# Kernel optimization log

Hardware: AMD Instinct MI355X
Metric: run time of the kernel (lower is better)

## Reference

```python
import jax, jax.numpy as jnp
import numpy as np

MIN_PS = 4
MAX_PS = 16


def _enforce(mb):
    # mb: (L,) bool candidate boundaries (merge_signal < 0.7-quantile)
    # Faithful re-implementation of _enforce_patch_size_constraints:
    # walk boundaries left->right, skip segments < MIN_PS (start not advanced),
    # accept otherwise, and insert ceil(ps/MAX_PS)-1 evenly spaced splits for
    # oversized segments. seq_len-1 is always appended as a candidate.
    L = mb.shape[0]
    pos = jnp.arange(L, dtype=jnp.int32)
    cand = mb | (pos == L - 1)

    def fwd_step(start, inp):
        p, is_c = inp
        ps = p - start
        acc = is_c & (ps >= MIN_PS)
        k = jnp.where(acc, (ps + MAX_PS - 1) // MAX_PS, jnp.int32(1))
        sz = jnp.maximum(jnp.where(acc, ps // k, jnp.int32(1)), 1)
        new_start = jnp.where(acc, p, start)
        return new_start, (acc, start, sz, k)

    _, (acc, seg_start, sz, k) = jax.lax.scan(fwd_step, jnp.int32(0), (pos, cand))

    # Reverse scan: propagate each accepted boundary's (start, split_size, num_splits)
    # back to the interior positions of its segment so splits can be placed in parallel.
    def rev_step(carry, inp):
        a, s, z, kk = inp
        cs, cz, ck, cv = carry
        out = (cs, cz, ck, cv)
        ncarry = (jnp.where(a, s, cs), jnp.where(a, z, cz), jnp.where(a, kk, ck), cv | a)
        return ncarry, out

    init = (jnp.int32(0), jnp.int32(1), jnp.int32(1), jnp.bool_(False))
    _, (fs, fz, fk, fv) = jax.lax.scan(rev_step, init, (acc, seg_start, sz, k), reverse=True)
    r = pos - fs
    j = r // fz
    split = fv & (r > 0) & (r % fz == 0) & (j >= 1) & (j <= fk - 1)
    return acc | split


def reference(x, attention_mask, W1, b1, W2, b2, Wc, bc, Wb1, bb1, Wb2, bb2):
    B, L, D = x.shape
    # content scorer: Linear -> ReLU -> Linear -> Sigmoid
    content = jax.nn.sigmoid(jax.nn.relu(x @ W1 + b1) @ W2 + b2)[..., 0]  # (B, L)
    # grouped Conv1d(d, d//2, k=3, pad=1, groups=d//4)
    xc = jnp.transpose(x, (0, 2, 1))  # (B, D, L)
    pf = jax.lax.conv_general_dilated(xc, Wc, (1,), ((1, 1),),
                                      feature_group_count=D // 4,
                                      dimension_numbers=('NCH', 'OIH', 'NCH'))
    pf = jnp.transpose(pf + bc[None, :, None], (0, 2, 1))  # (B, L, D//2)
    comb = jnp.concatenate([x, pf], axis=-1)
    bscore = jax.nn.sigmoid(jax.nn.relu(comb @ Wb1 + bb1) @ Wb2 + bb2)[..., 0]  # (B, L)
    signal = content * (1.0 - bscore) * attention_mask
    thr = jnp.quantile(signal, 0.7, axis=1, keepdims=True)
    mb = signal < thr
    new_b = jax.vmap(_enforce)(mb)  # (B, L) bool, new_b[:,0] is always False

    # segment id per token = inclusive cumsum of boundaries
    seg = jnp.cumsum(new_b.astype(jnp.int32), axis=1)
    seg_flat = (seg + jnp.arange(B, dtype=jnp.int32)[:, None] * L).reshape(-1)
    NS = B * L
    xm = x * attention_mask[..., None]
    e = jnp.sum(xm * xm, axis=-1).reshape(-1)  # softmax logits = ||token||^2
    m = jax.ops.segment_max(e, seg_flat, num_segments=NS)
    w = jnp.exp(e - m[seg_flat])
    denom = jax.ops.segment_sum(w, seg_flat, num_segments=NS)
    wn = w / denom[seg_flat]
    merged = jax.ops.segment_sum(xm.reshape(-1, D) * wn[:, None], seg_flat,
                                 num_segments=NS).reshape(B, L, D)
    # segment_boundaries: 1 for every segment except the first, zero padding
    n_last = seg[:, -1]
    p = jnp.arange(L)
    seg_bounds = ((p[None, :] >= 1) & (p[None, :] <= n_last[:, None])).astype(jnp.float32)
    return merged, seg_bounds


def setup_inputs() -> dict:
    key = jax.random.key(0)
    B, L, D = 4, 8192, 512
    ks = jax.random.split(key, 8)
    s = 0.02
    return {
        'x': jax.random.normal(ks[0], (B, L, D), jnp.float32),
        'attention_mask': jnp.ones((B, L), jnp.float32),
        'W1': jax.random.normal(ks[1], (D, D // 4), jnp.float32) * s,
        'b1': jnp.zeros((D // 4,), jnp.float32),
        'W2': jax.random.normal(ks[2], (D // 4, 1), jnp.float32) * s,
        'b2': jnp.zeros((1,), jnp.float32),
        'Wc': jax.random.normal(ks[3], (D // 2, 4, 3), jnp.float32) * s,
        'bc': jnp.zeros((D // 2,), jnp.float32),
        'Wb1': jax.random.normal(ks[4], (D + D // 2, D // 4), jnp.float32) * s,
        'bb1': jnp.zeros((D // 4,), jnp.float32),
        'Wb2': jax.random.normal(ks[5], (D // 4, 1), jnp.float32) * s,
        'bb2': jnp.zeros((1,), jnp.float32),
    }
```

## Files before the change

kernel.cpp:

```cpp
#include <hip/hip_runtime.h>
#include <math.h>

#define B_  4
#define L_  8192
#define D_  512
#define BL_ (B_*L_)
#define TOK 64
#define XS  68
#define KC  16
#define NCH (D_/KC)

__global__ __launch_bounds__(256, 2) void k_signal(
    const float* __restrict__ x, const float* __restrict__ mask,
    const float* __restrict__ W1, const float* __restrict__ b1,
    const float* __restrict__ W2, const float* __restrict__ b2,
    const float* __restrict__ Wc, const float* __restrict__ bc,
    const float* __restrict__ Wb1, const float* __restrict__ bb1,
    const float* __restrict__ Wb2, const float* __restrict__ bb2,
    float* __restrict__ signal, float* __restrict__ e)
{
  __shared__ float ws1[KC][128];
  __shared__ float wsb[KC][128];
  __shared__ float wsp[8][128];
  __shared__ float xt[KC][XS];
  __shared__ float pf[8][XS];

  const int t   = threadIdx.x;
  const int blk = blockIdx.x;
  const int b   = blk >> 7;
  const int l0  = (blk & 127) << 6;
  const float* xb = x + (size_t)b * L_ * D_;

  const int jq = t & 31, tw = t >> 5;
  const int j0 = jq << 2, tok0 = tw << 3;

  const int stok = t >> 2, skk = t & 3;
  const int oo_c = t >> 5;
  const int m2   = (t & 31) << 1;
  const int cb_c = (oo_c >> 1) << 2;

  const int srow = t >> 5, sc4 = (t & 31) << 2;

  float a1[8][4], a2[8][4];
#pragma unroll
  for (int i = 0; i < 8; ++i)
#pragma unroll
    for (int j = 0; j < 4; ++j) { a1[i][j] = 0.f; a2[i][j] = 0.f; }
  float esacc = 0.f;

  float4 r_w1a, r_w1b, r_wba, r_wbb, r_wp, r_xv, r_hv;
  float4 r_wc0, r_wc1, r_wc2;
  float  r_bc;

  auto LOAD = [&](int c) {
    const int kc = c << 4;
    r_w1a = *reinterpret_cast<const float4*>(W1  + (size_t)(kc + srow) * 128 + sc4);
    r_w1b = *reinterpret_cast<const float4*>(W1  + (size_t)(kc + 8 + srow) * 128 + sc4);
    r_wba = *reinterpret_cast<const float4*>(Wb1 + (size_t)(kc + srow) * 128 + sc4);
    r_wbb = *reinterpret_cast<const float4*>(Wb1 + (size_t)(kc + 8 + srow) * 128 + sc4);
    r_wp  = *reinterpret_cast<const float4*>(Wb1 + (size_t)(512 + (c << 3) + srow) * 128 + sc4);
    r_xv  = *reinterpret_cast<const float4*>(xb + (size_t)(l0 + stok) * D_ + kc + (skk << 2));
    if (t < 8) {
      const int hh = t >> 2, kk = t & 3;
      const int l = hh ? (l0 + TOK) : (l0 - 1);
      r_hv = make_float4(0.f, 0.f, 0.f, 0.f);
      if (l >= 0 && l < L_)
        r_hv = *reinterpret_cast<const float4*>(xb + (size_t)l * D_ + kc + (kk << 2));
    }
    const int o = (c << 3) + oo_c;
    const float* wcp = Wc + o * 12;
    r_wc0 = *reinterpret_cast<const float4*>(wcp);
    r_wc1 = *reinterpret_cast<const float4*>(wcp + 4);
    r_wc2 = *reinterpret_cast<const float4*>(wcp + 8);
    r_bc  = bc[o];
  };

  LOAD(0);

  for (int c = 0; c < NCH; ++c) {
    __syncthreads();

    *reinterpret_cast<float4*>(&ws1[srow][sc4])     = r_w1a;
    *reinterpret_cast<float4*>(&ws1[8 + srow][sc4]) = r_w1b;
    *reinterpret_cast<float4*>(&wsb[srow][sc4])     = r_wba;
    *reinterpret_cast<float4*>(&wsb[8 + srow][sc4]) = r_wbb;
    *reinterpret_cast<float4*>(&wsp[srow][sc4])     = r_wp;
    {
      const float4 v = r_xv;
      esacc = fmaf(v.x, v.x, esacc); esacc = fmaf(v.y, v.y, esacc);
      esacc = fmaf(v.z, v.z, esacc); esacc = fmaf(v.w, v.w, esacc);
      const int r = skk << 2;
      xt[r + 0][stok] = v.x; xt[r + 1][stok] = v.y;
      xt[r + 2][stok] = v.z; xt[r + 3][stok] = v.w;
    }
    if (t < 8) {
      const int hh = t >> 2, kk = t & 3;
      const int col = TOK + hh, r = kk << 2;
      xt[r + 0][col] = r_hv.x; xt[r + 1][col] = r_hv.y;
      xt[r + 2][col] = r_hv.z; xt[r + 3][col] = r_hv.w;
    }
    __syncthreads();

    float wcl[12];
    wcl[0] = r_wc0.x; wcl[1]  = r_wc0.y; wcl[2]  = r_wc0.z; wcl[3]  = r_wc0.w;
    wcl[4] = r_wc1.x; wcl[5]  = r_wc1.y; wcl[6]  = r_wc1.z; wcl[7]  = r_wc1.w;
    wcl[8] = r_wc2.x; wcl[9]  = r_wc2.y; wcl[10] = r_wc2.z; wcl[11] = r_wc2.w;
    const float bcv = r_bc;

    if (c + 1 < NCH) LOAD(c + 1);

    {
      float pa = bcv, pb = bcv;
      const int tm1 = (m2 == 0) ? TOK : m2 - 1;
      const int tp2 = (m2 + 2 == TOK) ? TOK + 1 : m2 + 2;
#pragma unroll
      for (int i = 0; i < 4; ++i) {
        const float* row = &xt[cb_c + i][0];
        const float  xm1 = row[tm1];
        const float2 x01 = *reinterpret_cast<const float2*>(&row[m2]);
        const float  xp2 = row[tp2];
        pa = fmaf(xm1,   wcl[i * 3 + 0], pa);
        pa = fmaf(x01.x, wcl[i * 3 + 1], pa);
        pa = fmaf(x01.y, wcl[i * 3 + 2], pa);
        pb = fmaf(x01.x, wcl[i * 3 + 0], pb);
        pb = fmaf(x01.y, wcl[i * 3 + 1], pb);
        pb = fmaf(xp2,   wcl[i * 3 + 2], pb);
      }
      *reinterpret_cast<float2*>(&pf[oo_c][m2]) = make_float2(pa, pb);
    }

#pragma unroll 4
    for (int k = 0; k < KC; ++k) {
      const float4 w1 = *reinterpret_cast<const float4*>(&ws1[k][j0]);
      const float4 wb = *reinterpret_cast<const float4*>(&wsb[k][j0]);
      const float4 xa = *reinterpret_cast<const float4*>(&xt[k][tok0]);
      const float4 xc = *reinterpret_cast<const float4*>(&xt[k][tok0 + 4]);
      const float xs8[8] = {xa.x, xa.y, xa.z, xa.w, xc.x, xc.y, xc.z, xc.w};
#pragma unroll
      for (int i = 0; i < 8; ++i) {
        a1[i][0] = fmaf(xs8[i], w1.x, a1[i][0]);
        a1[i][1] = fmaf(xs8[i], w1.y, a1[i][1]);
        a1[i][2] = fmaf(xs8[i], w1.z, a1[i][2]);
        a1[i][3] = fmaf(xs8[i], w1.w, a1[i][3]);
        a2[i][0] = fmaf(xs8[i], wb.x, a2[i][0]);
        a2[i][1] = fmaf(xs8[i], wb.y, a2[i][1]);
        a2[i][2] = fmaf(xs8[i], wb.z, a2[i][2]);
        a2[i][3] = fmaf(xs8[i], wb.w, a2[i][3]);
      }
    }
    __syncthreads();

#pragma unroll 2
    for (int oo = 0; oo < 8; ++oo) {
      const float4 wp = *reinterpret_cast<const float4*>(&wsp[oo][j0]);
      const float4 pa4 = *reinterpret_cast<const float4*>(&pf[oo][tok0]);
      const float4 pb4 = *reinterpret_cast<const float4*>(&pf[oo][tok0 + 4]);
      const float ps8[8] = {pa4.x, pa4.y, pa4.z, pa4.w, pb4.x, pb4.y, pb4.z, pb4.w};
#pragma unroll
      for (int i = 0; i < 8; ++i) {
        a2[i][0] = fmaf(ps8[i], wp.x, a2[i][0]);
        a2[i][1] = fmaf(ps8[i], wp.y, a2[i][1]);
        a2[i][2] = fmaf(ps8[i], wp.z, a2[i][2]);
        a2[i][3] = fmaf(ps8[i], wp.w, a2[i][3]);
      }
    }
  }

  {
    float b1v[4], w2v[4], bbv[4], wv2[4];
#pragma unroll
    for (int jj = 0; jj < 4; ++jj) {
      b1v[jj] = b1[j0 + jj];  w2v[jj] = W2[j0 + jj];
      bbv[jj] = bb1[j0 + jj]; wv2[jj] = Wb2[j0 + jj];
    }
    const float bias2 = b2[0], biasb2 = bb2[0];
#pragma unroll
    for (int i = 0; i < 8; ++i) {
      float p1 = 0.f, p2 = 0.f;
#pragma unroll
      for (int jj = 0; jj < 4; ++jj) {
        const float h1 = a1[i][jj] + b1v[jj];
        if (h1 > 0.f) p1 = fmaf(h1, w2v[jj], p1);
        const float h2 = a2[i][jj] + bbv[jj];
        if (h2 > 0.f) p2 = fmaf(h2, wv2[jj], p2);
      }
#pragma unroll
      for (int off = 1; off < 32; off <<= 1) {
        p1 += __shfl_xor(p1, off, 64);
        p2 += __shfl_xor(p2, off, 64);
      }
      if (jq == 0) {
        const int gi = b * L_ + l0 + tok0 + i;
        const float content = 1.f / (1.f + expf(-(p1 + bias2)));
        const float bscore  = 1.f / (1.f + expf(-(p2 + biasb2)));
        signal[gi] = content * (1.f - bscore) * mask[gi];
      }
    }
  }

  {
    float es = esacc;
    es += __shfl_xor(es, 1, 64);
    es += __shfl_xor(es, 2, 64);
    if (skk == 0) {
      const int gi = b * L_ + l0 + stok;
      const float m = mask[gi];
      e[gi] = m * m * es;
    }
  }
}

__device__ __forceinline__ int chain_sim(unsigned long long w, int from) {
  int last = -1;
  while (from < 64) {
    const unsigned long long m = w & (~0ull << from);
    if (m == 0ull) break;
    const int p = __ffsll(m) - 1;
    last = p;
    from = p + 4;
  }
  return last;
}

__global__ __launch_bounds__(1024) void k_select(
    const float* __restrict__ signal,
    int* __restrict__ starts, int* __restrict__ nlast, float* __restrict__ bounds)
{
  __shared__ unsigned int bins[4][256];
  __shared__ unsigned int sel_prefix;
  __shared__ int sel_rank;
  __shared__ float sh_thr;
  __shared__ unsigned int wmin[16];
  __shared__ int wcnt[16];
  __shared__ unsigned long long cw[128];
  __shared__ unsigned char nb[L_];
  __shared__ signed char tbl[128][4];
  __shared__ int st_in[128];
  __shared__ int tsum[256];
  __shared__ int offs[257];

  const int b = blockIdx.x, t = threadIdx.x;
  const int wv = t >> 6, lane = t & 63;
  const float* s = signal + b * L_;

  float val[8];
  unsigned int key[8];
#pragma unroll
  for (int i = 0; i < 8; ++i) {
    val[i] = s[(i << 10) + t];
    const unsigned int u = __float_as_uint(val[i]);
    key[i] = (u & 0x80000000u) ? ~u : (u | 0x80000000u);
  }

  if (t == 0) { sel_prefix = 0u; sel_rank = 5733; }
  __syncthreads();
  for (int round = 0; round < 4; ++round) {
    reinterpret_cast<unsigned int*>(bins)[t] = 0u;
    __syncthreads();
    const unsigned int pre = sel_prefix;
    const int shift = 24 - 8 * round;
#pragma unroll
    for (int i = 0; i < 8; ++i) {
      if (round == 0 || (key[i] >> (shift + 8)) == pre)
        atomicAdd(&bins[t >> 8][(key[i] >> shift) & 255u], 1u);
    }
    __syncthreads();
    if (t < 256)
      bins[0][t] = bins[0][t] + bins[1][t] + bins[2][t] + bins[3][t];
    __syncthreads();
    if (t < 64) {
      const unsigned int c0 = bins[0][(t << 2) + 0], c1 = bins[0][(t << 2) + 1];
      const unsigned int c2 = bins[0][(t << 2) + 2], c3 = bins[0][(t << 2) + 3];
      const unsigned int lsum = c0 + c1 + c2 + c3;
      unsigned int run = lsum;
#pragma unroll
      for (int off = 1; off < 64; off <<= 1) {
        const unsigned int v = __shfl_up(run, off, 64);
        if (t >= off) run += v;
      }
      const int r = sel_rank;
      if (r >= (int)(run - lsum) && r < (int)run) {
        int rr = r - (int)(run - lsum);
        unsigned int cbin;
        if (rr < (int)c0) { cbin = 0; }
        else if (rr < (int)(c0 + c1)) { cbin = 1; rr -= (int)c0; }
        else if (rr < (int)(c0 + c1 + c2)) { cbin = 2; rr -= (int)(c0 + c1); }
        else { cbin = 3; rr -= (int)(c0 + c1 + c2); }
        sel_rank = rr;
        sel_prefix = (pre << 8) | ((unsigned int)(t << 2) | cbin);
      }
    }
    __syncthreads();
  }
  const unsigned int k0 = sel_prefix;

  {
    int cle = 0;
    unsigned int mgt = 0xFFFFFFFFu;
#pragma unroll
    for (int i = 0; i < 8; ++i) {
      if (key[i] <= k0) ++cle;
      else mgt = min(mgt, key[i]);
    }
#pragma unroll
    for (int off = 1; off < 64; off <<= 1) {
      cle += __shfl_xor(cle, off, 64);
      mgt = min(mgt, (unsigned int)__shfl_xor((int)mgt, off, 64));
    }
    if (lane == 0) { wcnt[wv] = cle; wmin[wv] = mgt; }
    __syncthreads();
    if (t == 0) {
      int C = 0; unsigned int M = 0xFFFFFFFFu;
      for (int g = 0; g < 16; ++g) { C += wcnt[g]; M = min(M, wmin[g]); }
      const unsigned int k1 = (C >= 5735) ? k0 : M;
      const unsigned int u0 = (k0 & 0x80000000u) ? (k0 & 0x7fffffffu) : ~k0;
      const unsigned int u1 = (k1 & 0x80000000u) ? (k1 & 0x7fffffffu) : ~k1;
      const float v0 = __uint_as_float(u0);
      const float v1 = __uint_as_float(u1);
      const float g = 0.7f * 8191.0f - 5733.0f;
      sh_thr = v0 + g * (v1 - v0);
    }
    __syncthreads();
  }
  const float thr = sh_thr;

#pragma unroll
  for (int i = 0; i < 8; ++i) {
    const unsigned long long m = __ballot(val[i] < thr);
    if (lane == 0) cw[(i << 4) + wv] = m;
  }
  {
    const int base = t << 3;
#pragma unroll
    for (int i = 0; i < 8; ++i) nb[base + i] = 0;
  }
  __syncthreads();
  if (t == 0) cw[127] |= (1ull << 63);
  __syncthreads();

  if (t < 512) {
    const int blk = t >> 2, cls = t & 3;
    tbl[blk][cls] = (signed char)chain_sim(cw[blk], cls);
  }
  __syncthreads();

  if (t == 0) {
    int st = 0;
    for (int blk = 0; blk < 128; ++blk) {
      const int bs = blk << 6;
      st_in[blk] = st;
      int pl;
      if (blk == 0) {
        pl = chain_sim(cw[0], 4);
      } else {
        int off = st + 4 - bs;
        if (off < 0) off = 0;
        pl = tbl[blk][off];
      }
      if (pl >= 0) st = bs + pl;
    }
  }
  __syncthreads();

  if (t < 128) {
    const int bs = t << 6;
    const unsigned long long w = cw[t];
    int st = st_in[t];
    int from = st + 4 - bs;
    if (from < 0) from = 0;
    while (from < 64) {
      const unsigned long long m = w & (~0ull << from);
      if (m == 0ull) break;
      const int p_rel = __ffsll(m) - 1;
      const int p = bs + p_rel;
      nb[p] = 1;
      const int ps = p - st;
      const int k = (ps + 15) >> 4;
      if (k > 1) {
        int sz = ps / k; if (sz < 1) sz = 1;
        for (int j = 1; j < k; ++j) nb[st + j * sz] = 1;
      }
      st = p;
      from = p_rel + 4;
    }
  }
  __syncthreads();

  if (t < 256) {
    const int base = t << 5;
    int ls = 0;
    for (int i = 0; i < 32; ++i) ls += nb[base + i];
    tsum[t] = ls;
  }
  __syncthreads();
  if (t == 0) {
    int r = 0;
    for (int i = 0; i < 256; ++i) { offs[i] = r; r += tsum[i]; }
    offs[256] = r;
  }
  __syncthreads();
  if (t < 256) {
    const int base = t << 5;
    int run = offs[t];
    for (int i = 0; i < 32; ++i) {
      run += nb[base + i];
      if (nb[base + i]) starts[b * L_ + run] = base + i;
    }
  }
  if (t == 0) { starts[b * L_ + 0] = 0; nlast[b] = offs[256]; }
  __syncthreads();
  const int total = offs[256];
  for (int i = t; i < L_; i += 1024)
    bounds[b * L_ + i] = (i >= 1 && i <= total) ? 1.0f : 0.0f;
}

__global__ __launch_bounds__(256) void k_merge(const float* __restrict__ x,
    const float* __restrict__ mask, const float* __restrict__ e,
    const int* __restrict__ starts, const int* __restrict__ nlast,
    float* __restrict__ merged)
{
  const int idx = (blockIdx.x << 2) + (threadIdx.x >> 6);
  const int b   = idx >> 13;
  const int sid = idx & (L_ - 1);
  const int n = nlast[b];
  const int lane = threadIdx.x & 63;
  const int c0 = lane << 3;
  float* o = merged + (size_t)(b * L_ + sid) * D_ + c0;
  if (sid > n) {
    const float4 z = make_float4(0.f, 0.f, 0.f, 0.f);
    reinterpret_cast<float4*>(o)[0] = z;
    reinterpret_cast<float4*>(o)[1] = z;
    return;
  }
  const int t0 = starts[b * L_ + sid];
  const int t1 = (sid < n) ? starts[b * L_ + sid + 1] : L_;
  const int len = t1 - t0;
  const float* eb = e + b * L_;

  float acc[8] = {0,0,0,0,0,0,0,0};

  if (len <= 64) {
    const float ev = (lane < len) ? eb[t0 + lane] : -INFINITY;
    float mx = ev;
#pragma unroll
    for (int off = 1; off < 64; off <<= 1)
      mx = fmaxf(mx, __shfl_xor(mx, off, 64));
    const float ex = expf(ev - mx);
    float den = ex;
#pragma unroll
    for (int off = 1; off < 64; off <<= 1)
      den += __shfl_xor(den, off, 64);
    const float mk = (lane < len) ? mask[b * L_ + t0 + lane] : 0.f;
    const float scl = (ex / den) * mk;

    const float* xr = x + (size_t)(b * L_ + t0) * D_ + c0;
    float4 u0 = reinterpret_cast<const float4*>(xr)[0];
    float4 u1 = reinterpret_cast<const float4*>(xr)[1];
    for (int r = 0; r < len; ++r) {
      float4 n0, n1;
      if (r + 1 < len) {
        const float* xn = xr + (size_t)(r + 1) * D_;
        n0 = reinterpret_cast<const float4*>(xn)[0];
        n1 = reinterpret_cast<const float4*>(xn)[1];
      }
      const float sc = __shfl(scl, r, 64);
      acc[0] = fmaf(sc, u0.x, acc[0]); acc[1] = fmaf(sc, u0.y, acc[1]);
      acc[2] = fmaf(sc, u0.z, acc[2]); acc[3] = fmaf(sc, u0.w, acc[3]);
      acc[4] = fmaf(sc, u1.x, acc[4]); acc[5] = fmaf(sc, u1.y, acc[5]);
      acc[6] = fmaf(sc, u1.z, acc[6]); acc[7] = fmaf(sc, u1.w, acc[7]);
      u0 = n0; u1 = n1;
    }
  } else {
    float mx = -INFINITY;
    for (int p = t0; p < t1; ++p) mx = fmaxf(mx, eb[p]);
    float den = 0.f;
    for (int p = t0; p < t1; ++p) den += expf(eb[p] - mx);
    for (int p = t0; p < t1; ++p) {
      const float wn = expf(eb[p] - mx) / den;
      const float sc = wn * mask[b * L_ + p];
      const float* xr = x + ((size_t)(b * L_ + p)) * D_ + c0;
      const float4 u0 = reinterpret_cast<const float4*>(xr)[0];
      const float4 u1 = reinterpret_cast<const float4*>(xr)[1];
      acc[0] = fmaf(sc, u0.x, acc[0]); acc[1] = fmaf(sc, u0.y, acc[1]);
      acc[2] = fmaf(sc, u0.z, acc[2]); acc[3] = fmaf(sc, u0.w, acc[3]);
      acc[4] = fmaf(sc, u1.x, acc[4]); acc[5] = fmaf(sc, u1.y, acc[5]);
      acc[6] = fmaf(sc, u1.z, acc[6]); acc[7] = fmaf(sc, u1.w, acc[7]);
    }
  }
  reinterpret_cast<float4*>(o)[0] = make_float4(acc[0], acc[1], acc[2], acc[3]);
  reinterpret_cast<float4*>(o)[1] = make_float4(acc[4], acc[5], acc[6], acc[7]);
}

extern "C" void kernel_launch(void* const* d_in, const int* in_sizes, int n_in,
                              void* d_out, int out_size, void* d_ws, size_t ws_size,
                              hipStream_t stream) {
  (void)in_sizes; (void)n_in; (void)out_size; (void)ws_size;
  const float* x    = (const float*)d_in[0];
  const float* mask = (const float*)d_in[1];
  const float* W1   = (const float*)d_in[2];
  const float* b1   = (const float*)d_in[3];
  const float* W2   = (const float*)d_in[4];
  const float* b2   = (const float*)d_in[5];
  const float* Wc   = (const float*)d_in[6];
  const float* bc   = (const float*)d_in[7];
  const float* Wb1  = (const float*)d_in[8];
  const float* bb1  = (const float*)d_in[9];
  const float* Wb2  = (const float*)d_in[10];
  const float* bb2  = (const float*)d_in[11];

  float* merged = (float*)d_out;
  float* bounds = (float*)d_out + (size_t)BL_ * D_;

  char* ws = (char*)d_ws;
  float* signal = (float*)(ws);
  float* e      = (float*)(ws + (size_t)BL_ * 4);
  int*   starts = (int*)  (ws + (size_t)BL_ * 8);
  int*   nlast  = (int*)  (ws + (size_t)BL_ * 12);

  k_signal<<<BL_ / TOK, 256, 0, stream>>>(x, mask, W1, b1, W2, b2, Wc, bc,
                                          Wb1, bb1, Wb2, bb2, signal, e);
  k_select<<<B_, 1024, 0, stream>>>(signal, starts, nlast, bounds);
  k_merge<<<BL_ / 4, 256, 0, stream>>>(x, mask, e, starts, nlast, merged);
}
```

Measured before the change: 303.0 us.

## Keep conv projection weights in registers, parallelize prefix scan, move bounds write to merge

In k_signal the conv-feature projection weights are now loaded straight into registers (8 float4 per thread) instead of being staged through shared memory. The grouped conv is computed by 128 threads producing 4 outputs each from a float4 load. In k_select the serial 256-element prefix sum is replaced by a wavefront shuffle scan plus a small cross-wave add. The segment-bounds output is now written by k_merge rather than the single-block-per-batch k_select. Together these shorten the serial tail of k_select and cut shared traffic in k_signal, at the cost of higher register pressure under launch_bounds(256,2).

```diff
diff --git a/kernel.cpp b/kernel.cpp
--- a/kernel.cpp
+++ b/kernel.cpp
@@ -21,7 +21,6 @@
 {
   __shared__ float ws1[KC][128];
   __shared__ float wsb[KC][128];
-  __shared__ float wsp[8][128];
   __shared__ float xt[KC][XS];
   __shared__ float pf[8][XS];
 
@@ -35,8 +34,8 @@
   const int j0 = jq << 2, tok0 = tw << 3;
 
   const int stok = t >> 2, skk = t & 3;
-  const int oo_c = t >> 5;
-  const int m2   = (t & 31) << 1;
+  const int oo_c = (t >> 4) & 7;
+  const int tokq = (t & 15) << 2;
   const int cb_c = (oo_c >> 1) << 2;
 
   const int srow = t >> 5, sc4 = (t & 31) << 2;
@@ -48,7 +47,8 @@
     for (int j = 0; j < 4; ++j) { a1[i][j] = 0.f; a2[i][j] = 0.f; }
   float esacc = 0.f;
 
-  float4 r_w1a, r_w1b, r_wba, r_wbb, r_wp, r_xv, r_hv;
+  float4 r_w1a, r_w1b, r_wba, r_wbb, r_xv, r_hv;
+  float4 r_wp[8];
   float4 r_wc0, r_wc1, r_wc2;
   float  r_bc;
 
@@ -58,7 +58,12 @@
     r_w1b = *reinterpret_cast<const float4*>(W1  + (size_t)(kc + 8 + srow) * 128 + sc4);
     r_wba = *reinterpret_cast<const float4*>(Wb1 + (size_t)(kc + srow) * 128 + sc4);
     r_wbb = *reinterpret_cast<const float4*>(Wb1 + (size_t)(kc + 8 + srow) * 128 + sc4);
-    r_wp  = *reinterpret_cast<const float4*>(Wb1 + (size_t)(512 + (c << 3) + srow) * 128 + sc4);
+    {
+      const float* wpg = Wb1 + (size_t)(512 + (c << 3)) * 128 + j0;
+#pragma unroll
+      for (int oo = 0; oo < 8; ++oo)
+        r_wp[oo] = *reinterpret_cast<const float4*>(wpg + (oo << 7));
+    }
     r_xv  = *reinterpret_cast<const float4*>(xb + (size_t)(l0 + stok) * D_ + kc + (skk << 2));
     if (t < 8) {
       const int hh = t >> 2, kk = t & 3;
@@ -84,7 +89,6 @@
     *reinterpret_cast<float4*>(&ws1[8 + srow][sc4]) = r_w1b;
     *reinterpret_cast<float4*>(&wsb[srow][sc4])     = r_wba;
     *reinterpret_cast<float4*>(&wsb[8 + srow][sc4]) = r_wbb;
-    *reinterpret_cast<float4*>(&wsp[srow][sc4])     = r_wp;
     {
       const float4 v = r_xv;
       esacc = fmaf(v.x, v.x, esacc); esacc = fmaf(v.y, v.y, esacc);
@@ -106,27 +110,27 @@
     wcl[4] = r_wc1.x; wcl[5]  = r_wc1.y; wcl[6]  = r_wc1.z; wcl[7]  = r_wc1.w;
     wcl[8] = r_wc2.x; wcl[9]  = r_wc2.y; wcl[10] = r_wc2.z; wcl[11] = r_wc2.w;
     const float bcv = r_bc;
+    float4 wpl[8];
+#pragma unroll
+    for (int oo = 0; oo < 8; ++oo) wpl[oo] = r_wp[oo];
 
     if (c + 1 < NCH) LOAD(c + 1);
 
-    {
-      float pa = bcv, pb = bcv;
-      const int tm1 = (m2 == 0) ? TOK : m2 - 1;
-      const int tp2 = (m2 + 2 == TOK) ? TOK + 1 : m2 + 2;
+    if (t < 128) {
+      float p0 = bcv, p1 = bcv, p2 = bcv, p3 = bcv;
 #pragma unroll
       for (int i = 0; i < 4; ++i) {
         const float* row = &xt[cb_c + i][0];
-        const float  xm1 = row[tm1];
-        const float2 x01 = *reinterpret_cast<const float2*>(&row[m2]);
-        const float  xp2 = row[tp2];
-        pa = fmaf(xm1,   wcl[i * 3 + 0], pa);
-        pa = fmaf(x01.x, wcl[i * 3 + 1], pa);
-        pa = fmaf(x01.y, wcl[i * 3 + 2], pa);
-        pb = fmaf(x01.x, wcl[i * 3 + 0], pb);
-        pb = fmaf(x01.y, wcl[i * 3 + 1], pb);
-        pb = fmaf(xp2,   wcl[i * 3 + 2], pb);
-      }
-      *reinterpret_cast<float2*>(&pf[oo_c][m2]) = make_float2(pa, pb);
+        const float  xm1 = (tokq == 0) ? row[TOK] : row[tokq - 1];
+        const float4 x4  = *reinterpret_cast<const float4*>(&row[tokq]);
+        const float  xp4 = (tokq == 60) ? row[TOK + 1] : row[tokq + 4];
+        const float w0 = wcl[i * 3 + 0], w1 = wcl[i * 3 + 1], w2 = wcl[i * 3 + 2];
+        p0 = fmaf(xm1,  w0, p0); p0 = fmaf(x4.x, w1, p0); p0 = fmaf(x4.y, w2, p0);
+        p1 = fmaf(x4.x, w0, p1); p1 = fmaf(x4.y, w1, p1); p1 = fmaf(x4.z, w2, p1);
+        p2 = fmaf(x4.y, w0, p2); p2 = fmaf(x4.z, w1, p2); p2 = fmaf(x4.w, w2, p2);
+        p3 = fmaf(x4.z, w0, p3); p3 = fmaf(x4.w, w1, p3); p3 = fmaf(xp4,  w2, p3);
+      }
+      *reinterpret_cast<float4*>(&pf[oo_c][tokq]) = make_float4(p0, p1, p2, p3);
     }
 
 #pragma unroll 4
@@ -150,9 +154,9 @@
     }
     __syncthreads();
 
-#pragma unroll 2
+#pragma unroll
     for (int oo = 0; oo < 8; ++oo) {
-      const float4 wp = *reinterpret_cast<const float4*>(&wsp[oo][j0]);
+      const float4 wp = wpl[oo];
       const float4 pa4 = *reinterpret_cast<const float4*>(&pf[oo][tok0]);
       const float4 pb4 = *reinterpret_cast<const float4*>(&pf[oo][tok0 + 4]);
       const float ps8[8] = {pa4.x, pa4.y, pa4.z, pa4.w, pb4.x, pb4.y, pb4.z, pb4.w};
@@ -224,7 +228,7 @@
 
 __global__ __launch_bounds__(1024) void k_select(
     const float* __restrict__ signal,
-    int* __restrict__ starts, int* __restrict__ nlast, float* __restrict__ bounds)
+    int* __restrict__ starts, int* __restrict__ nlast)
 {
   __shared__ unsigned int bins[4][256];
   __shared__ unsigned int sel_prefix;
@@ -236,7 +240,6 @@
   __shared__ unsigned char nb[L_];
   __shared__ signed char tbl[128][4];
   __shared__ int st_in[128];
-  __shared__ int tsum[256];
   __shared__ int offs[257];
 
   const int b = blockIdx.x, t = threadIdx.x;
@@ -386,44 +389,52 @@
   }
   __syncthreads();
 
+  int ls = 0, run = 0;
   if (t < 256) {
     const int base = t << 5;
-    int ls = 0;
     for (int i = 0; i < 32; ++i) ls += nb[base + i];
-    tsum[t] = ls;
-  }
-  __syncthreads();
-  if (t == 0) {
-    int r = 0;
-    for (int i = 0; i < 256; ++i) { offs[i] = r; r += tsum[i]; }
-    offs[256] = r;
+    run = ls;
+#pragma unroll
+    for (int off = 1; off < 64; off <<= 1) {
+      const int v = __shfl_up(run, off, 64);
+      if ((t & 63) >= off) run += v;
+    }
+    if ((t & 63) == 63) wcnt[t >> 6] = run;
+  }
+  __syncthreads();
+  if (t < 256) {
+    const int w = t >> 6;
+    int addb = 0;
+    if (w > 0) addb += wcnt[0];
+    if (w > 1) addb += wcnt[1];
+    if (w > 2) addb += wcnt[2];
+    offs[t] = addb + run - ls;
+    if (t == 255) offs[256] = addb + run;
   }
   __syncthreads();
   if (t < 256) {
     const int base = t << 5;
-    int run = offs[t];
+    int rn = offs[t];
     for (int i = 0; i < 32; ++i) {
-      run += nb[base + i];
-      if (nb[base + i]) starts[b * L_ + run] = base + i;
+      rn += nb[base + i];
+      if (nb[base + i]) starts[b * L_ + rn] = base + i;
     }
   }
   if (t == 0) { starts[b * L_ + 0] = 0; nlast[b] = offs[256]; }
-  __syncthreads();
-  const int total = offs[256];
-  for (int i = t; i < L_; i += 1024)
-    bounds[b * L_ + i] = (i >= 1 && i <= total) ? 1.0f : 0.0f;
 }
 
 __global__ __launch_bounds__(256) void k_merge(const float* __restrict__ x,
     const float* __restrict__ mask, const float* __restrict__ e,
     const int* __restrict__ starts, const int* __restrict__ nlast,
-    float* __restrict__ merged)
+    float* __restrict__ merged, float* __restrict__ bounds)
 {
   const int idx = (blockIdx.x << 2) + (threadIdx.x >> 6);
   const int b   = idx >> 13;
   const int sid = idx & (L_ - 1);
   const int n = nlast[b];
   const int lane = threadIdx.x & 63;
+  if (lane == 0)
+    bounds[(size_t)b * L_ + sid] = (sid >= 1 && sid <= n) ? 1.0f : 0.0f;
   const int c0 = lane << 3;
   float* o = merged + (size_t)(b * L_ + sid) * D_ + c0;
   if (sid > n) {
@@ -519,6 +530,6 @@
 
   k_signal<<<BL_ / TOK, 256, 0, stream>>>(x, mask, W1, b1, W2, b2, Wc, bc,
                                           Wb1, bb1, Wb2, bb2, signal, e);
-  k_select<<<B_, 1024, 0, stream>>>(signal, starts, nlast, bounds);
-  k_merge<<<BL_ / 4, 256, 0, stream>>>(x, mask, e, starts, nlast, merged);
+  k_select<<<B_, 1024, 0, stream>>>(signal, starts, nlast);
+  k_merge<<<BL_ / 4, 256, 0, stream>>>(x, mask, e, starts, nlast, merged, bounds);
 }
```

Measured after the change: 315.0 us. 1.04x slower.
